# Kernel optimization log

Hardware: AMD Instinct MI355X
Metric: run time of the kernel (lower is better)

Reference implementation:

```python
import jax, jax.numpy as jnp
import numpy as np

N = 8192       # nodes per graph
E = 262144     # edges per graph (avg degree 32)
H = 8          # attention heads
C = 128        # hidden dim per head (H*C = 1024 to match Linear(1024,128))
IN = 128       # input feature dim
NEG_SLOPE = 0.2


def _gat_conv(x, edge_index, W, att_src, att_dst, bias):
    """PyG GATConv (concat=True, add_self_loops=True, shared lin for src/dst)."""
    n = x.shape[0]
    loop = jnp.arange(n, dtype=edge_index.dtype)
    src = jnp.concatenate([edge_index[0], loop])  # [E+N]
    dst = jnp.concatenate([edge_index[1], loop])
    h = (x @ W).reshape(n, H, C)                         # [N,H,C]
    a_src = jnp.sum(h * att_src, axis=-1)                # [N,H]
    a_dst = jnp.sum(h * att_dst, axis=-1)                # [N,H]
    e = jax.nn.leaky_relu(a_src[src] + a_dst[dst], NEG_SLOPE)   # [E+N,H]
    m = jax.ops.segment_max(e, dst, num_segments=n)      # per-dst max for stability
    ex = jnp.exp(e - m[dst])
    den = jax.ops.segment_sum(ex, dst, num_segments=n)
    alpha = ex / den[dst]                                # [E+N,H] neighborhood softmax
    out = jax.ops.segment_sum(h[src] * alpha[:, :, None], dst, num_segments=n)
    return out.reshape(n, H * C) + bias                  # [N, H*C]


def setup_inputs() -> dict:
    key = jax.random.key(0)
    ks = jax.random.split(key, 12)
    s = 0.05  # keep activations in a sane range
    return {
        "x1": jax.random.normal(ks[0], (N, IN), jnp.float32),
        "edge_index1": jax.random.randint(ks[1], (2, E), 0, N, dtype=jnp.int64),
        "W1": jax.random.normal(ks[2], (IN, H * C), jnp.float32) * s,
        "att_src1": jax.random.normal(ks[3], (H, C), jnp.float32) * s,
        "att_dst1": jax.random.normal(ks[4], (H, C), jnp.float32) * s,
        "b1": jnp.zeros((H * C,), jnp.float32),
        "x2": jax.random.normal(ks[5], (N, IN), jnp.float32),
        "edge_index2": jax.random.randint(ks[6], (2, E), 0, N, dtype=jnp.int64),
        "W2": jax.random.normal(ks[7], (IN, H * C), jnp.float32) * s,
        "att_src2": jax.random.normal(ks[8], (H, C), jnp.float32) * s,
        "att_dst2": jax.random.normal(ks[9], (H, C), jnp.float32) * s,
        "b2": jnp.zeros((H * C,), jnp.float32),
        "Wl": jax.random.normal(ks[10], (H * C, 128), jnp.float32) * s,
        "bl": jnp.zeros((128,), jnp.float32),
    }


def reference(x1, edge_index1, W1, att_src1, att_dst1, b1,
              x2, edge_index2, W2, att_src2, att_dst2, b2, Wl, bl):
    emb1 = _gat_conv(x1, edge_index1, W1, att_src1, att_dst1, b1)  # [N1,1024]
    emb2 = _gat_conv(x2, edge_index2, W2, att_src2, att_dst2, b2)  # [N2,1024]
    scores = emb1 @ emb2.T                                          # [N1,N2]
    w1 = jax.nn.softmax(scores, axis=1)
    w2 = jax.nn.softmax(scores, axis=0)
    cross1 = (w2 @ emb2) @ Wl + bl      # [N1,128]
    cross2 = (w1.T @ emb1) @ Wl + bl    # [N2,128]
    return (jnp.mean(cross1, axis=0), jnp.mean(cross2, axis=0))
```

## Files before the change

### kernel.cpp

```cpp
#include <hip/hip_runtime.h>


#define NN 8192
#define EE 262144
#define NEG 0.2f

#define BKT 128
#define RNG (NN / BKT)
#define CAP 2560
#define EB  128
#define CHK (EE / EB)

#define U_CNT   0
#define U_G     (U_CNT + 4*BKT)
#define U_MEMB  (U_G + 2048)
#define U_ZEND  (U_MEMB + 2048)
#define U_U     (U_ZEND)
#define U_ASRC  (U_U + 2*2048)
#define U_ADST  (U_ASRC + 2*NN*8)
#define U_PR    (U_ADST + 2*NN*8)
#define U_WACC  (U_PR + 2*NN*16)
#define U_BIND  (U_WACC + 2*NN*8)
#define U_BINS  (U_BIND + 2*BKT*CAP)
#define ZERO_BYTES ((size_t)U_ZEND * 4)

__global__ __launch_bounds__(256) void k_u(
    const float* __restrict__ W1, const float* __restrict__ as1, const float* __restrict__ ad1,
    const float* __restrict__ W2, const float* __restrict__ as2, const float* __restrict__ ad2,
    float* __restrict__ u) {
  int b = blockIdx.x;
  int graph = b >> 4, sd = (b >> 3) & 1, head = b & 7;
  const float* W = graph ? W2 : W1;
  const float* att = graph ? (sd ? ad2 : as2) : (sd ? ad1 : as1);
  int w = threadIdx.x >> 6, lane = threadIdx.x & 63;
  float2 av = ((const float2*)(att + head * 128))[lane];
  float* uo = u + graph * 2048 + sd * 1024 + head * 128;
#pragma unroll 4
  for (int k = w; k < 128; k += 4) {
    float2 wv = ((const float2*)(W + (size_t)k * 1024 + head * 128))[lane];
    float p = av.x * wv.x + av.y * wv.y;
    p += __shfl_xor(p, 1);  p += __shfl_xor(p, 2);  p += __shfl_xor(p, 4);
    p += __shfl_xor(p, 8);  p += __shfl_xor(p, 16); p += __shfl_xor(p, 32);
    if (lane == 0) uo[k] = p;
  }
}

__global__ __launch_bounds__(256) void k_a(
    const float* __restrict__ x1, const float* __restrict__ x2,
    const float* __restrict__ u, float* __restrict__ asrc, float* __restrict__ adst) {
  int graph = blockIdx.y;
  const float* x = graph ? x2 : x1;
  const float* ug = u + graph * 2048;
  __shared__ float xs[64][129];
  __shared__ float us[16][128];
  int t = threadIdx.x;
  for (int i = t; i < 2048; i += 256) us[i >> 7][i & 127] = ug[i];
  int n0 = blockIdx.x * 64;
  const float* xb = x + (size_t)n0 * 128;
  for (int i = t; i < 64 * 128; i += 256) xs[i >> 7][i & 127] = xb[i];
  __syncthreads();
  int nl = t & 63;
  int j0 = (t >> 6) * 4;
  float a0 = 0.f, a1 = 0.f, a2 = 0.f, a3 = 0.f;
#pragma unroll 4
  for (int k = 0; k < 128; ++k) {
    float xv = xs[nl][k];
    a0 += xv * us[j0 + 0][k];
    a1 += xv * us[j0 + 1][k];
    a2 += xv * us[j0 + 2][k];
    a3 += xv * us[j0 + 3][k];
  }
  int n = n0 + nl;
  float* outp = (j0 < 8) ? (asrc + graph * (NN * 8) + n * 8 + j0)
                         : (adst + graph * (NN * 8) + n * 8 + (j0 - 8));
  outp[0] = a0; outp[1] = a1; outp[2] = a2; outp[3] = a3;
}

__global__ __launch_bounds__(512) void k_bin(
    const int* __restrict__ ei1, const int* __restrict__ ei2,
    int* __restrict__ cnt, int* __restrict__ binD, int* __restrict__ binS) {
  int g = blockIdx.y;
  const int* ei = g ? ei2 : ei1;
  __shared__ int hD[BKT], hS[BKT], bD[BKT], bS[BKT], cD[BKT], cS[BKT];
  int t = threadIdx.x;
  for (int i = t; i < BKT; i += 512) { hD[i] = 0; hS[i] = 0; cD[i] = 0; cS[i] = 0; }
  __syncthreads();
  int e0 = blockIdx.x * CHK;
  for (int i = t; i < CHK; i += 512) {
    int s = ei[e0 + i], d = ei[EE + e0 + i];
    atomicAdd(&hD[d >> 6], 1);
    atomicAdd(&hS[s >> 6], 1);
  }
  __syncthreads();
  for (int i = t; i < BKT; i += 512) {
    bD[i] = atomicAdd(cnt + (2 * g + 0) * BKT + i, hD[i]);
    bS[i] = atomicAdd(cnt + (2 * g + 1) * BKT + i, hS[i]);
  }
  __syncthreads();
  int* bdg = binD + (size_t)g * BKT * CAP;
  int* bsg = binS + (size_t)g * BKT * CAP;
  for (int i = t; i < CHK; i += 512) {
    int s = ei[e0 + i], d = ei[EE + e0 + i];
    int kb = d >> 6;
    int p = bD[kb] + atomicAdd(&cD[kb], 1);
    bdg[kb * CAP + p] = (s << 6) | (d & 63);
    kb = s >> 6;
    p = bS[kb] + atomicAdd(&cS[kb], 1);
    bsg[kb * CAP + p] = (d << 6) | (s & 63);
  }
}

__global__ __launch_bounds__(512) void k_den_red(
    const int* __restrict__ cnt, const int* __restrict__ binD,
    const float* __restrict__ asrc, const float* __restrict__ adst,
    float* __restrict__ pr) {
  int g = blockIdx.y, b = blockIdx.x;
  int lo = b * RNG;
  const float* as = asrc + g * (NN * 8);
  const float* ad = adst + g * (NN * 8);
  float2* prg = (float2*)pr + (size_t)g * (NN * 8);
  __shared__ float den[RNG * 8];
  __shared__ float adsts[RNG * 8];
  int t = threadIdx.x;
  for (int i = t; i < RNG * 8; i += 512) {
    float avv = ad[lo * 8 + i];
    float v = as[lo * 8 + i] + avv;
    v = v > 0.f ? v : NEG * v;
    adsts[i] = avv;
    den[i] = __expf(v);
  }
  __syncthreads();
  int n = cnt[(2 * g + 0) * BKT + b];
  const int* recs = binD + (size_t)g * BKT * CAP + b * CAP;
  int rid = t >> 3, h = t & 7;
  for (int base = 0; base < n; base += 256) {
    int rv[4]; bool ok[4]; float sv[4];
#pragma unroll
    for (int uu = 0; uu < 4; ++uu) {
      int i = base + uu * 64 + rid;
      ok[uu] = i < n;
      rv[uu] = ok[uu] ? recs[i] : 0;
    }
#pragma unroll
    for (int uu = 0; uu < 4; ++uu)
      sv[uu] = ok[uu] ? as[(rv[uu] >> 6) * 8 + h] : 0.f;
#pragma unroll
    for (int uu = 0; uu < 4; ++uu) {
      if (ok[uu]) {
        int dl = rv[uu] & 63;
        float v = sv[uu] + adsts[dl * 8 + h];
        v = v > 0.f ? v : NEG * v;
        atomicAdd(&den[dl * 8 + h], __expf(v));
      }
    }
  }
  __syncthreads();
  for (int i = t; i < RNG * 8; i += 512)
    prg[lo * 8 + i] = make_float2(adsts[i], 1.0f / den[i]);
}

__global__ __launch_bounds__(512) void k_wacc_red(
    const int* __restrict__ cnt, const int* __restrict__ binS,
    const float* __restrict__ asrc, const float* __restrict__ pr,
    float* __restrict__ wacc) {
  int g = blockIdx.y, b = blockIdx.x;
  int lo = b * RNG;
  const float* as = asrc + g * (NN * 8);
  const float2* prg = (const float2*)pr + (size_t)g * (NN * 8);
  __shared__ float wv[RNG * 8];
  __shared__ float asrcs[RNG * 8];
  int t = threadIdx.x;
  for (int i = t; i < RNG * 8; i += 512) {
    float sva = as[lo * 8 + i];
    float2 f2 = prg[lo * 8 + i];
    float v = sva + f2.x;
    v = v > 0.f ? v : NEG * v;
    asrcs[i] = sva;
    wv[i] = __expf(v) * f2.y;
  }
  __syncthreads();
  int n = cnt[(2 * g + 1) * BKT + b];
  const int* recs = binS + (size_t)g * BKT * CAP + b * CAP;
  int rid = t >> 3, h = t & 7;
  for (int base = 0; base < n; base += 256) {
    int rv[4]; bool ok[4]; float2 pv[4];
#pragma unroll
    for (int uu = 0; uu < 4; ++uu) {
      int i = base + uu * 64 + rid;
      ok[uu] = i < n;
      rv[uu] = ok[uu] ? recs[i] : 0;
    }
#pragma unroll
    for (int uu = 0; uu < 4; ++uu)
      pv[uu] = ok[uu] ? prg[(size_t)(rv[uu] >> 6) * 8 + h] : make_float2(0.f, 0.f);
#pragma unroll
    for (int uu = 0; uu < 4; ++uu) {
      if (ok[uu]) {
        int sl = rv[uu] & 63;
        float v = asrcs[sl * 8 + h] + pv[uu].x;
        v = v > 0.f ? v : NEG * v;
        atomicAdd(&wv[sl * 8 + h], __expf(v) * pv[uu].y);
      }
    }
  }
  __syncthreads();
  for (int i = t; i < RNG * 8; i += 512)
    wacc[g * (NN * 8) + lo * 8 + i] = wv[i];
}

#define GCHUNK 128
__global__ __launch_bounds__(256) void k_gred(
    const float* __restrict__ x1, const float* __restrict__ x2,
    const float* __restrict__ wacc, float* __restrict__ g) {
  int graph = blockIdx.y;
  const float* x = graph ? x2 : x1;
  const float* w = wacc + graph * (NN * 8);
  float* gg = g + graph * 1024;
  int t = threadIdx.x;
  int k = t & 127;
  int h0 = (t >> 7) * 4;
  int n0 = blockIdx.x * GCHUNK;
  float a0 = 0.f, a1 = 0.f, a2 = 0.f, a3 = 0.f;
#pragma unroll 4
  for (int n = n0; n < n0 + GCHUNK; ++n) {
    float xv = x[(size_t)n * 128 + k];
    float4 wv4 = *(const float4*)(w + (size_t)n * 8 + h0);
    a0 += xv * wv4.x; a1 += xv * wv4.y; a2 += xv * wv4.z; a3 += xv * wv4.w;
  }
  atomicAdd(gg + (h0 + 0) * 128 + k, a0);
  atomicAdd(gg + (h0 + 1) * 128 + k, a1);
  atomicAdd(gg + (h0 + 2) * 128 + k, a2);
  atomicAdd(gg + (h0 + 3) * 128 + k, a3);
}

__global__ __launch_bounds__(256) void k_memb(
    const float* __restrict__ W1, const float* __restrict__ W2,
    const float* __restrict__ b1, const float* __restrict__ b2,
    const float* __restrict__ g, float* __restrict__ memb) {
  int graph = blockIdx.z;
  int kc = blockIdx.y;
  const float* W = graph ? W2 : W1;
  const float* b = graph ? b2 : b1;
  int e = blockIdx.x * 256 + threadIdx.x;
  int head = e >> 7;
  const float* gr = g + graph * 1024 + head * 128;
  float s = 0.f;
#pragma unroll
  for (int k = kc * 16; k < kc * 16 + 16; ++k) s += gr[k] * W[(size_t)k * 1024 + e];
  s *= (1.0f / (float)NN);
  if (kc == 0) s += b[e];
  atomicAdd(memb + graph * 1024 + e, s);
}

__global__ __launch_bounds__(256) void k_out(
    const float* __restrict__ memb, const float* __restrict__ Wl,
    const float* __restrict__ bl, float* __restrict__ out) {
  int t = threadIdx.x;
  int j = t & 127;
  int k0 = blockIdx.x * 32;
  const float* m = (t < 128) ? (memb + 1024) : memb;
  float s = 0.f;
#pragma unroll
  for (int k = k0; k < k0 + 32; ++k) s += m[k] * Wl[(size_t)k * 128 + j];
  if (blockIdx.x == 0) s += bl[j];
  atomicAdd(out + t, s);
}

extern "C" void kernel_launch(void* const* d_in, const int* in_sizes, int n_in,
                              void* d_out, int out_size, void* d_ws, size_t ws_size,
                              hipStream_t stream) {
  const float* x1  = (const float*)d_in[0];
  const int*   ei1 = (const int*)d_in[1];
  const float* W1  = (const float*)d_in[2];
  const float* as1 = (const float*)d_in[3];
  const float* ad1 = (const float*)d_in[4];
  const float* b1  = (const float*)d_in[5];
  const float* x2  = (const float*)d_in[6];
  const int*   ei2 = (const int*)d_in[7];
  const float* W2  = (const float*)d_in[8];
  const float* as2 = (const float*)d_in[9];
  const float* ad2 = (const float*)d_in[10];
  const float* b2  = (const float*)d_in[11];
  const float* Wl  = (const float*)d_in[12];
  const float* bl  = (const float*)d_in[13];
  float* out = (float*)d_out;

  int*   cnt  = (int*)d_ws + U_CNT;
  float* g    = (float*)d_ws + U_G;
  float* memb = (float*)d_ws + U_MEMB;
  float* u    = (float*)d_ws + U_U;
  float* asrc = (float*)d_ws + U_ASRC;
  float* adst = (float*)d_ws + U_ADST;
  float* pr   = (float*)d_ws + U_PR;
  float* wacc = (float*)d_ws + U_WACC;
  int*   binD = (int*)d_ws + U_BIND;
  int*   binS = (int*)d_ws + U_BINS;

  hipMemsetAsync(d_ws, 0, ZERO_BYTES, stream);
  hipMemsetAsync(d_out, 0, (size_t)out_size * 4, stream);

  k_bin<<<dim3(EB, 2), 512, 0, stream>>>(ei1, ei2, cnt, binD, binS);
  k_u<<<32, 256, 0, stream>>>(W1, as1, ad1, W2, as2, ad2, u);
  k_a<<<dim3(NN / 64, 2), 256, 0, stream>>>(x1, x2, u, asrc, adst);
  k_den_red<<<dim3(BKT, 2), 512, 0, stream>>>(cnt, binD, asrc, adst, pr);
  k_wacc_red<<<dim3(BKT, 2), 512, 0, stream>>>(cnt, binS, asrc, pr, wacc);
  k_gred<<<dim3(NN / GCHUNK, 2), 256, 0, stream>>>(x1, x2, wacc, g);
  k_memb<<<dim3(4, 8, 2), 256, 0, stream>>>(W1, W2, b1, b2, g, memb);
  k_out<<<32, 256, 0, stream>>>(memb, Wl, bl, out);
}
```

Baseline: 190.3 us.

## Stage edge bins in LDS and vectorize per-edge head loads in reductions

The binning kernel now keeps its edge chunk in registers, computes per-bucket prefix sums, and sorts records locally in shared memory so each bucket is written to global memory contiguously instead of as scattered per-edge stores. The two edge reductions switch from one thread per (edge, head) to one thread per edge that loads all 8 heads with float4 loads, using head-major shared arrays to cut bank conflicts on the atomics. GCHUNK is doubled in the gradient-reduce kernel. In exchange, the binning kernel uses more shared memory and runs a serial scan with many barriers, and the per-edge threads now do 8 atomics each.

```diff
diff --git a/kernel.cpp b/kernel.cpp
--- a/kernel.cpp
+++ b/kernel.cpp
@@ -81,32 +81,57 @@
     int* __restrict__ cnt, int* __restrict__ binD, int* __restrict__ binS) {
   int g = blockIdx.y;
   const int* ei = g ? ei2 : ei1;
-  __shared__ int hD[BKT], hS[BKT], bD[BKT], bS[BKT], cD[BKT], cS[BKT];
-  int t = threadIdx.x;
-  for (int i = t; i < BKT; i += 512) { hD[i] = 0; hS[i] = 0; cD[i] = 0; cS[i] = 0; }
+  __shared__ int hD[BKT], hS[BKT], scD[BKT], scS[BKT];
+  __shared__ int cD[BKT], cS[BKT], bD[BKT], bS[BKT];
+  __shared__ int ldsD[CHK], ldsS[CHK];
+  __shared__ unsigned char kbAD[CHK], kbAS[CHK];
+  int t = threadIdx.x;
+  if (t < BKT) { hD[t] = 0; cD[t] = 0; }
+  else if (t < 2 * BKT) { int i = t - BKT; hS[i] = 0; cS[i] = 0; }
   __syncthreads();
   int e0 = blockIdx.x * CHK;
-  for (int i = t; i < CHK; i += 512) {
-    int s = ei[e0 + i], d = ei[EE + e0 + i];
-    atomicAdd(&hD[d >> 6], 1);
-    atomicAdd(&hS[s >> 6], 1);
-  }
-  __syncthreads();
-  for (int i = t; i < BKT; i += 512) {
-    bD[i] = atomicAdd(cnt + (2 * g + 0) * BKT + i, hD[i]);
-    bS[i] = atomicAdd(cnt + (2 * g + 1) * BKT + i, hS[i]);
+  int sv[4], dv[4];
+#pragma unroll
+  for (int k = 0; k < 4; ++k) {
+    sv[k] = ei[e0 + t + k * 512];
+    dv[k] = ei[EE + e0 + t + k * 512];
+    atomicAdd(&hD[dv[k] >> 6], 1);
+    atomicAdd(&hS[sv[k] >> 6], 1);
+  }
+  __syncthreads();
+  if (t < BKT) { scD[t] = hD[t]; bD[t] = atomicAdd(cnt + (2 * g + 0) * BKT + t, hD[t]); }
+  else if (t < 2 * BKT) { int i = t - BKT; scS[i] = hS[i]; bS[i] = atomicAdd(cnt + (2 * g + 1) * BKT + i, hS[i]); }
+  __syncthreads();
+  for (int o = 1; o < BKT; o <<= 1) {
+    int v = 0;
+    if (t < BKT) { if (t >= o) v = scD[t - o]; }
+    else if (t < 2 * BKT) { int i = t - BKT; if (i >= o) v = scS[i - o]; }
+    __syncthreads();
+    if (t < BKT) scD[t] += v;
+    else if (t < 2 * BKT) scS[t - BKT] += v;
+    __syncthreads();
+  }
+#pragma unroll
+  for (int k = 0; k < 4; ++k) {
+    int kb = dv[k] >> 6;
+    int pos = (scD[kb] - hD[kb]) + atomicAdd(&cD[kb], 1);
+    ldsD[pos] = (sv[k] << 6) | (dv[k] & 63);
+    kbAD[pos] = (unsigned char)kb;
+    kb = sv[k] >> 6;
+    pos = (scS[kb] - hS[kb]) + atomicAdd(&cS[kb], 1);
+    ldsS[pos] = (dv[k] << 6) | (sv[k] & 63);
+    kbAS[pos] = (unsigned char)kb;
   }
   __syncthreads();
   int* bdg = binD + (size_t)g * BKT * CAP;
   int* bsg = binS + (size_t)g * BKT * CAP;
-  for (int i = t; i < CHK; i += 512) {
-    int s = ei[e0 + i], d = ei[EE + e0 + i];
-    int kb = d >> 6;
-    int p = bD[kb] + atomicAdd(&cD[kb], 1);
-    bdg[kb * CAP + p] = (s << 6) | (d & 63);
-    kb = s >> 6;
-    p = bS[kb] + atomicAdd(&cS[kb], 1);
-    bsg[kb * CAP + p] = (d << 6) | (s & 63);
+#pragma unroll
+  for (int k = 0; k < 4; ++k) {
+    int i = t + k * 512;
+    int kb = kbAD[i];
+    bdg[kb * CAP + bD[kb] + (i - (scD[kb] - hD[kb]))] = ldsD[i];
+    kb = kbAS[i];
+    bsg[kb * CAP + bS[kb] + (i - (scS[kb] - hS[kb]))] = ldsS[i];
   }
 }
 
@@ -119,44 +144,53 @@
   const float* as = asrc + g * (NN * 8);
   const float* ad = adst + g * (NN * 8);
   float2* prg = (float2*)pr + (size_t)g * (NN * 8);
-  __shared__ float den[RNG * 8];
-  __shared__ float adsts[RNG * 8];
-  int t = threadIdx.x;
-  for (int i = t; i < RNG * 8; i += 512) {
-    float avv = ad[lo * 8 + i];
-    float v = as[lo * 8 + i] + avv;
+  __shared__ float den[8][RNG];
+  __shared__ float adsts[8][RNG];
+  int t = threadIdx.x;
+  {
+    int dl = t & 63, h = t >> 6;
+    float avv = ad[(lo + dl) * 8 + h];
+    float v = as[(lo + dl) * 8 + h] + avv;
     v = v > 0.f ? v : NEG * v;
-    adsts[i] = avv;
-    den[i] = __expf(v);
+    adsts[h][dl] = avv;
+    den[h][dl] = __expf(v);
   }
   __syncthreads();
   int n = cnt[(2 * g + 0) * BKT + b];
   const int* recs = binD + (size_t)g * BKT * CAP + b * CAP;
-  int rid = t >> 3, h = t & 7;
-  for (int base = 0; base < n; base += 256) {
-    int rv[4]; bool ok[4]; float sv[4];
-#pragma unroll
-    for (int uu = 0; uu < 4; ++uu) {
-      int i = base + uu * 64 + rid;
-      ok[uu] = i < n;
-      rv[uu] = ok[uu] ? recs[i] : 0;
-    }
-#pragma unroll
-    for (int uu = 0; uu < 4; ++uu)
-      sv[uu] = ok[uu] ? as[(rv[uu] >> 6) * 8 + h] : 0.f;
-#pragma unroll
-    for (int uu = 0; uu < 4; ++uu) {
-      if (ok[uu]) {
-        int dl = rv[uu] & 63;
-        float v = sv[uu] + adsts[dl * 8 + h];
-        v = v > 0.f ? v : NEG * v;
-        atomicAdd(&den[dl * 8 + h], __expf(v));
+  for (int base = 0; base < n; base += 2048) {
+    int rv[4]; bool ok[4]; float4 q0[4], q1[4];
+#pragma unroll
+    for (int k = 0; k < 4; ++k) {
+      int i = base + k * 512 + t;
+      ok[k] = i < n;
+      rv[k] = ok[k] ? recs[i] : 0;
+    }
+#pragma unroll
+    for (int k = 0; k < 4; ++k) {
+      const float4* p = (const float4*)(as + (size_t)(rv[k] >> 6) * 8);
+      if (ok[k]) { q0[k] = p[0]; q1[k] = p[1]; }
+    }
+#pragma unroll
+    for (int k = 0; k < 4; ++k) {
+      if (ok[k]) {
+        int dl = rv[k] & 63;
+        float e[8] = {q0[k].x, q0[k].y, q0[k].z, q0[k].w,
+                      q1[k].x, q1[k].y, q1[k].z, q1[k].w};
+#pragma unroll
+        for (int h = 0; h < 8; ++h) {
+          float v = e[h] + adsts[h][dl];
+          v = v > 0.f ? v : NEG * v;
+          atomicAdd(&den[h][dl], __expf(v));
+        }
       }
     }
   }
   __syncthreads();
-  for (int i = t; i < RNG * 8; i += 512)
-    prg[lo * 8 + i] = make_float2(adsts[i], 1.0f / den[i]);
+  {
+    int dl = t >> 3, h = t & 7;
+    prg[lo * 8 + t] = make_float2(adsts[h][dl], 1.0f / den[h][dl]);
+  }
 }
 
 __global__ __launch_bounds__(512) void k_wacc_red(
@@ -167,48 +201,59 @@
   int lo = b * RNG;
   const float* as = asrc + g * (NN * 8);
   const float2* prg = (const float2*)pr + (size_t)g * (NN * 8);
-  __shared__ float wv[RNG * 8];
-  __shared__ float asrcs[RNG * 8];
-  int t = threadIdx.x;
-  for (int i = t; i < RNG * 8; i += 512) {
-    float sva = as[lo * 8 + i];
-    float2 f2 = prg[lo * 8 + i];
+  __shared__ float wv[8][RNG];
+  __shared__ float asrcs[8][RNG];
+  int t = threadIdx.x;
+  {
+    int sl = t & 63, h = t >> 6;
+    float sva = as[(lo + sl) * 8 + h];
+    float2 f2 = prg[(lo + sl) * 8 + h];
     float v = sva + f2.x;
     v = v > 0.f ? v : NEG * v;
-    asrcs[i] = sva;
-    wv[i] = __expf(v) * f2.y;
+    asrcs[h][sl] = sva;
+    wv[h][sl] = __expf(v) * f2.y;
   }
   __syncthreads();
   int n = cnt[(2 * g + 1) * BKT + b];
   const int* recs = binS + (size_t)g * BKT * CAP + b * CAP;
-  int rid = t >> 3, h = t & 7;
-  for (int base = 0; base < n; base += 256) {
-    int rv[4]; bool ok[4]; float2 pv[4];
-#pragma unroll
-    for (int uu = 0; uu < 4; ++uu) {
-      int i = base + uu * 64 + rid;
-      ok[uu] = i < n;
-      rv[uu] = ok[uu] ? recs[i] : 0;
-    }
-#pragma unroll
-    for (int uu = 0; uu < 4; ++uu)
-      pv[uu] = ok[uu] ? prg[(size_t)(rv[uu] >> 6) * 8 + h] : make_float2(0.f, 0.f);
-#pragma unroll
-    for (int uu = 0; uu < 4; ++uu) {
-      if (ok[uu]) {
-        int sl = rv[uu] & 63;
-        float v = asrcs[sl * 8 + h] + pv[uu].x;
-        v = v > 0.f ? v : NEG * v;
-        atomicAdd(&wv[sl * 8 + h], __expf(v) * pv[uu].y);
+  for (int base = 0; base < n; base += 2048) {
+    int rv[4]; bool ok[4]; float4 q0[4], q1[4], q2[4], q3[4];
+#pragma unroll
+    for (int k = 0; k < 4; ++k) {
+      int i = base + k * 512 + t;
+      ok[k] = i < n;
+      rv[k] = ok[k] ? recs[i] : 0;
+    }
+#pragma unroll
+    for (int k = 0; k < 4; ++k) {
+      const float4* p = (const float4*)(prg + (size_t)(rv[k] >> 6) * 8);
+      if (ok[k]) { q0[k] = p[0]; q1[k] = p[1]; q2[k] = p[2]; q3[k] = p[3]; }
+    }
+#pragma unroll
+    for (int k = 0; k < 4; ++k) {
+      if (ok[k]) {
+        int sl = rv[k] & 63;
+        float a[8] = {q0[k].x, q0[k].z, q1[k].x, q1[k].z,
+                      q2[k].x, q2[k].z, q3[k].x, q3[k].z};
+        float r[8] = {q0[k].y, q0[k].w, q1[k].y, q1[k].w,
+                      q2[k].y, q2[k].w, q3[k].y, q3[k].w};
+#pragma unroll
+        for (int h = 0; h < 8; ++h) {
+          float v = asrcs[h][sl] + a[h];
+          v = v > 0.f ? v : NEG * v;
+          atomicAdd(&wv[h][sl], __expf(v) * r[h]);
+        }
       }
     }
   }
   __syncthreads();
-  for (int i = t; i < RNG * 8; i += 512)
-    wacc[g * (NN * 8) + lo * 8 + i] = wv[i];
-}
-
-#define GCHUNK 128
+  {
+    int sl = t >> 3, h = t & 7;
+    wacc[g * (NN * 8) + lo * 8 + t] = wv[h][sl];
+  }
+}
+
+#define GCHUNK 256
 __global__ __launch_bounds__(256) void k_gred(
     const float* __restrict__ x1, const float* __restrict__ x2,
     const float* __restrict__ wacc, float* __restrict__ g) {
```

After: 202.2 us. 6.3% more time.
